# Optimization experiments

Measured on AMD Instinct MI355X. Metric: run time of the kernel, lower is better.

The kernel has to match this reference:

```python
import jax, jax.numpy as jnp
import numpy as np
import math

N_HEADS = 16

def _rope_tables(T, D, dtype):
    # inv_freq over even dims, emb = [freqs, freqs] -> [T, D]
    inv_freq = 1.0 / (10000.0 ** (jnp.arange(0, D, 2, dtype=jnp.float32) / D))
    freqs = jnp.arange(T, dtype=jnp.float32)[:, None] * inv_freq[None, :]  # [T, D/2]
    emb = jnp.concatenate([freqs, freqs], axis=-1)  # [T, D]
    return jnp.cos(emb).astype(dtype), jnp.sin(emb).astype(dtype)

def _rotate_half(x):
    d = x.shape[-1] // 2
    return jnp.concatenate([-x[..., d:], x[..., :d]], axis=-1)

def setup_inputs() -> dict:
    key = jax.random.key(0)
    ks = jax.random.split(key, 5)
    B, T, C = 2, 2048, 1024
    s = 1.0 / math.sqrt(C)
    return {
        "x": jax.random.normal(ks[0], (B, T, C), dtype=jnp.float32),
        "Wq": jax.random.normal(ks[1], (C, C), dtype=jnp.float32) * s,
        "Wk": jax.random.normal(ks[2], (C, C), dtype=jnp.float32) * s,
        "Wv": jax.random.normal(ks[3], (C, C), dtype=jnp.float32) * s,
        "Wo": jax.random.normal(ks[4], (C, C), dtype=jnp.float32) * s,
    }

def reference(x, Wq, Wk, Wv, Wo):
    B, T, C = x.shape
    H = N_HEADS
    D = C // H
    # QKV projections (torch Linear, bias=False: y = x @ W.T), split into heads
    def proj(W):
        return (x @ W.T).reshape(B, T, H, D).transpose(0, 2, 1, 3)  # [B,H,T,D]
    q, k, v = proj(Wq), proj(Wk), proj(Wv)
    # RoPE
    cos, sin = _rope_tables(T, D, x.dtype)  # [T,D] each, broadcast over B,H
    q = q * cos + _rotate_half(q) * sin
    k = k * cos + _rotate_half(k) * sin
    # scaled dot-product attention with causal mask
    scale = 1.0 / math.sqrt(D)
    attn = jnp.einsum('bhtd,bhsd->bhts', q, k) * scale  # [B,H,T,T]
    row = jnp.arange(T)[:, None]
    col = jnp.arange(T)[None, :]
    attn = jnp.where(col > row, -jnp.inf, attn)
    p = jax.nn.softmax(attn, axis=-1)
    out = jnp.einsum('bhts,bhsd->bhtd', p, v)  # [B,H,T,D]
    out = out.transpose(0, 2, 1, 3).reshape(B, T, C)
    return out @ Wo.T
```

## Files before the change

kernel.cpp:

```cpp
#include <hip/hip_runtime.h>
#include <hip/hip_bf16.h>


typedef __hip_bfloat16 bf16;
typedef __attribute__((ext_vector_type(8))) short bf16x8;
typedef __attribute__((ext_vector_type(4))) float f32x4;
typedef __attribute__((ext_vector_type(4))) short short4v;

#define MFMA16(a, b, c) __builtin_amdgcn_mfma_f32_16x16x32_bf16((a), (b), (c), 0, 0, 0)

constexpr int Bn = 2, Hn = 16, Tn = 2048, Dn = 64, Cn = 1024;
constexpr size_t NE = (size_t)Bn * Tn * Cn;
constexpr size_t WE = (size_t)Cn * Cn;
constexpr float QSCALE = 0.125f * 1.44269504088896f;
constexpr int PS = 68;

__device__ inline unsigned short bfbits(float x) {
    bf16 b = __float2bfloat16(x);
    return *(unsigned short*)&b;
}

__device__ inline bf16x8 pack8(f32x4 a, f32x4 b) {
    bf16x8 r;
#pragma unroll
    for (int i = 0; i < 4; ++i) r[i] = (short)bfbits(a[i]);
#pragma unroll
    for (int i = 0; i < 4; ++i) r[4 + i] = (short)bfbits(b[i]);
    return r;
}

__global__ __launch_bounds__(256) void convert_kernel(
    const float* __restrict__ x, const float* __restrict__ wq,
    const float* __restrict__ wk, const float* __restrict__ wv,
    const float* __restrict__ wo, bf16* __restrict__ dst)
{
    int blk = blockIdx.x;
    int lane = threadIdx.x & 63;
    int lx = lane & 15, quad = lane >> 4;
    const float* src;
    size_t doff;
    if (blk < 2048) {
        int frag = blk * 4 + (threadIdx.x >> 6);
        int mt = frag >> 5, kc = frag & 31;
        src = x + (size_t)(mt * 16 + lx) * Cn + kc * 32 + quad * 8;
        doff = (size_t)frag * 512 + lane * 8;
    } else {
        int w = (blk - 2048) >> 9, b = (blk - 2048) & 511;
        const float* s4[4] = {wq, wk, wv, wo};
        int frag = b * 4 + (threadIdx.x >> 6);
        int nb = frag >> 5, kc = frag & 31;
        src = s4[w] + (size_t)(nb * 16 + lx) * Cn + kc * 32 + quad * 8;
        doff = NE + (size_t)w * WE + (size_t)frag * 512 + lane * 8;
    }
    f32x4 a = *(const f32x4*)(src);
    f32x4 b2 = *(const f32x4*)(src + 4);
    *(bf16x8*)(dst + doff) = pack8(a, b2);
}

__global__ __launch_bounds__(256) void gemm_qkv_kernel(
    const bf16* __restrict__ Xf, const bf16* __restrict__ Wbase,
    bf16* __restrict__ Qo, bf16* __restrict__ Ko, bf16* __restrict__ Vo)
{
    const int bm = blockIdx.x, bn = blockIdx.y, wsel = blockIdx.z;
    const bf16* W = Wbase + (size_t)wsel * WE;
    const int tid  = threadIdx.x;
    const int wave = tid >> 6, lane = tid & 63;
    const int lx   = lane & 15, quad = lane >> 4;
    const int wm = wave >> 1, wn = wave & 1;

    const int mt0 = bm * 8 + wm * 4;
    const int nb0 = bn * 8 + wn * 4;
    const bf16* afrag = Xf + (size_t)mt0 * 32 * 512 + (size_t)lane * 8;
    const bf16* wfrag = W + (size_t)nb0 * 32 * 512 + (size_t)lane * 8;

    f32x4 acc[4][4] = {};
    bf16x8 acur[4], bcur[4], anxt[4], bnxt[4];
#pragma unroll
    for (int i = 0; i < 4; ++i) {
        acur[i] = *(const bf16x8*)(afrag + (size_t)i * 32 * 512);
        bcur[i] = *(const bf16x8*)(wfrag + (size_t)i * 32 * 512);
    }
    for (int kc = 0; kc < 32; ++kc) {
        if (kc < 31) {
#pragma unroll
            for (int i = 0; i < 4; ++i) {
                anxt[i] = *(const bf16x8*)(afrag + ((size_t)i * 32 + kc + 1) * 512);
                bnxt[i] = *(const bf16x8*)(wfrag + ((size_t)i * 32 + kc + 1) * 512);
            }
        }
#pragma unroll
        for (int mt = 0; mt < 4; ++mt)
#pragma unroll
            for (int nt = 0; nt < 4; ++nt)
                acc[mt][nt] = MFMA16(acur[mt], bcur[nt], acc[mt][nt]);
#pragma unroll
        for (int i = 0; i < 4; ++i) { acur[i] = anxt[i]; bcur[i] = bnxt[i]; }
    }

    const int h = bn * 2 + wn;
    if (wsel <= 1) {
#pragma unroll
        for (int mt = 0; mt < 4; ++mt)
#pragma unroll
            for (int r = 0; r < 4; ++r) {
                int mg = bm * 128 + wm * 64 + mt * 16 + quad * 4 + r;
                int t  = mg & (Tn - 1);
#pragma unroll
                for (int nt = 0; nt < 2; ++nt) {
                    int d = nt * 16 + lx;
                    float ang = (float)t * __expf(-(float)d * 0.2878231366f);
                    float c, s;
                    __sincosf(ang, &s, &c);
                    float a0 = acc[mt][nt][r], a1 = acc[mt][nt + 2][r];
                    acc[mt][nt][r]     = a0 * c - a1 * s;
                    acc[mt][nt + 2][r] = a1 * c + a0 * s;
                }
            }
    }

#pragma unroll
    for (int mt = 0; mt < 4; ++mt) {
        int mg0 = bm * 128 + wm * 64 + mt * 16 + quad * 4;
        int b = mg0 >> 11, tlo = mg0 & (Tn - 1);
        if (wsel == 0) {
#pragma unroll
            for (int nt = 0; nt < 4; ++nt)
#pragma unroll
                for (int r = 0; r < 4; ++r) {
                    int d = nt * 16 + lx;
                    Qo[((size_t)(b * Hn + h) * Tn + tlo + r) * Dn + d] =
                        __float2bfloat16(acc[mt][nt][r] * QSCALE);
                }
        } else if (wsel == 1) {
            bf16* Kf = Ko + (size_t)(b * Hn + h) * Tn * Dn;
            int c = tlo >> 6, ntk = (tlo >> 4) & 3;
#pragma unroll
            for (int nt = 0; nt < 4; ++nt) {
                size_t base = ((size_t)(c * 4 + ntk) * 2 + (nt >> 1)) * 512
                            + (size_t)((nt & 1) * 2 + (lx >> 3)) * 128
                            + (size_t)(tlo & 15) * 8 + (lx & 7);
#pragma unroll
                for (int r = 0; r < 4; ++r)
                    Kf[base + (size_t)r * 8] = __float2bfloat16(acc[mt][nt][r]);
            }
        } else {
            bf16* Vf = Vo + (size_t)(b * Hn + h) * Tn * Dn;
            int c = tlo >> 6, ksv = (tlo >> 5) & 1;
            int qv = (tlo >> 3) & 3, pos0 = tlo & 7;
#pragma unroll
            for (int nt = 0; nt < 4; ++nt) {
                short4v pk;
#pragma unroll
                for (int r = 0; r < 4; ++r) pk[r] = (short)bfbits(acc[mt][nt][r]);
                *(short4v*)&Vf[((size_t)(c * 8 + nt * 2 + ksv)) * 512
                               + (size_t)qv * 128 + (size_t)lx * 8 + pos0] = pk;
            }
        }
    }
}

__global__ __launch_bounds__(256) void gemm_out_kernel(
    const bf16* __restrict__ Af, const bf16* __restrict__ W, float* __restrict__ Out)
{
    const int bm = blockIdx.x, bn = blockIdx.y;
    const int tid  = threadIdx.x;
    const int wave = tid >> 6, lane = tid & 63;
    const int lx   = lane & 15, quad = lane >> 4;
    const int wm = wave >> 1, wn = wave & 1;

    const int mt0 = bm * 8 + wm * 4;
    const int nb0 = bn * 8 + wn * 4;
    const bf16* afrag = Af + (size_t)mt0 * 32 * 512 + (size_t)lane * 8;
    const bf16* wfrag = W + (size_t)nb0 * 32 * 512 + (size_t)lane * 8;

    f32x4 acc[4][4] = {};
    bf16x8 acur[4], bcur[4], anxt[4], bnxt[4];
#pragma unroll
    for (int i = 0; i < 4; ++i) {
        acur[i] = *(const bf16x8*)(afrag + (size_t)i * 32 * 512);
        bcur[i] = *(const bf16x8*)(wfrag + (size_t)i * 32 * 512);
    }
    for (int kc = 0; kc < 32; ++kc) {
        if (kc < 31) {
#pragma unroll
            for (int i = 0; i < 4; ++i) {
                anxt[i] = *(const bf16x8*)(afrag + ((size_t)i * 32 + kc + 1) * 512);
                bnxt[i] = *(const bf16x8*)(wfrag + ((size_t)i * 32 + kc + 1) * 512);
            }
        }
#pragma unroll
        for (int mt = 0; mt < 4; ++mt)
#pragma unroll
            for (int nt = 0; nt < 4; ++nt)
                acc[mt][nt] = MFMA16(acur[mt], bcur[nt], acc[mt][nt]);
#pragma unroll
        for (int i = 0; i < 4; ++i) { acur[i] = anxt[i]; bcur[i] = bnxt[i]; }
    }
#pragma unroll
    for (int mt = 0; mt < 4; ++mt)
#pragma unroll
        for (int nt = 0; nt < 4; ++nt)
#pragma unroll
            for (int r = 0; r < 4; ++r) {
                int mg = bm * 128 + wm * 64 + mt * 16 + quad * 4 + r;
                int ng = bn * 128 + wn * 64 + nt * 16 + lx;
                Out[(size_t)mg * Cn + ng] = acc[mt][nt][r];
            }
}

__global__ __launch_bounds__(256) void attn_kernel(
    const bf16* __restrict__ Q, const bf16* __restrict__ K,
    const bf16* __restrict__ Vt, bf16* __restrict__ O)
{
    __shared__ unsigned short Pl[4][16 * PS];
    const int f  = blockIdx.x;
    const int bh = (f & 7) * 4 + ((f >> 3) & 3);
    const int qb = 31 - (f >> 5);
    const int tid  = threadIdx.x;
    const int wave = tid >> 6, lane = tid & 63;
    const int lx   = lane & 15, quad = lane >> 4;

    const bf16* Qh = Q  + (size_t)bh * Tn * Dn;
    const bf16* Kh = K  + (size_t)bh * Tn * Dn;
    const bf16* Vh = Vt + (size_t)bh * Tn * Dn;
    unsigned short* pw = &Pl[wave][0];

    const int qrowA = qb * 64 + wave * 16 + lx;
    bf16x8 aq0 = *(const bf16x8*)(Qh + (size_t)qrowA * Dn + quad * 8);
    bf16x8 aq1 = *(const bf16x8*)(Qh + (size_t)qrowA * Dn + 32 + quad * 8);

    bf16x8 ones;
#pragma unroll
    for (int i = 0; i < 8; ++i) ones[i] = (short)0x3F80;

    f32x4 acc_o[4] = {};
    f32x4 acc_l = {};
    const int row_local = wave * 16 + quad * 4;

    auto load8 = [&](bf16x8* d, const bf16* p) {
#pragma unroll
        for (int i = 0; i < 8; ++i) d[i] = *(const bf16x8*)(p + (size_t)i * 512);
    };

    auto step = [&](const bf16x8* k, const bf16* vptr, bool diag) {
        bf16x8 v[8];
#pragma unroll
        for (int i = 0; i < 8; ++i) v[i] = *(const bf16x8*)(vptr + (size_t)i * 512);
        f32x4 accs[4] = {};
#pragma unroll
        for (int nt = 0; nt < 4; ++nt) {
            accs[nt] = MFMA16(aq0, k[nt * 2], accs[nt]);
            accs[nt] = MFMA16(aq1, k[nt * 2 + 1], accs[nt]);
        }
        if (!diag) {
#pragma unroll
            for (int nt = 0; nt < 4; ++nt)
#pragma unroll
                for (int r = 0; r < 4; ++r)
                    pw[(quad * 4 + r) * PS + nt * 16 + lx] = bfbits(exp2f(accs[nt][r]));
        } else {
#pragma unroll
            for (int nt = 0; nt < 4; ++nt) {
                int keyl = nt * 16 + lx;
#pragma unroll
                for (int r = 0; r < 4; ++r) {
                    float p2 = (keyl > row_local + r) ? 0.0f : exp2f(accs[nt][r]);
                    pw[(quad * 4 + r) * PS + nt * 16 + lx] = bfbits(p2);
                }
            }
        }
        asm volatile("s_waitcnt lgkmcnt(0)" ::: "memory");
        bf16x8 ap0 = *(const bf16x8*)&pw[lx * PS + quad * 8];
        bf16x8 ap1 = *(const bf16x8*)&pw[lx * PS + 32 + quad * 8];
        acc_l = MFMA16(ap0, ones, acc_l);
        acc_l = MFMA16(ap1, ones, acc_l);
#pragma unroll
        for (int dt = 0; dt < 4; ++dt) {
            acc_o[dt] = MFMA16(ap0, v[dt * 2], acc_o[dt]);
            acc_o[dt] = MFMA16(ap1, v[dt * 2 + 1], acc_o[dt]);
        }
    };

    const bf16* kp = Kh + lane * 8;
    const bf16* vp = Vh + lane * 8;

    bf16x8 ka[8], kb[8];
    load8(ka, kp);

    int ch = 0;
    while (ch + 1 <= qb) {
        load8(kb, kp + 4096);
        step(ka, vp, false);
        if (ch + 2 <= qb) load8(ka, kp + 8192);
        step(kb, vp + 4096, (ch + 1) == qb);
        kp += 8192; vp += 8192; ch += 2;
    }
    if (ch == qb)
        step(ka, vp, true);

    const int b = bh >> 4, h = bh & 15;
    const int mtile = b * 128 + qb * 4 + wave;
#pragma unroll
    for (int dt = 0; dt < 4; ++dt) {
        int ch2 = h * 64 + dt * 16 + lx;
        size_t base = ((size_t)mtile * 32 + (ch2 >> 5)) * 512
                    + (size_t)(((ch2 >> 3) & 3) * 16) * 8 + (ch2 & 7);
#pragma unroll
        for (int r = 0; r < 4; ++r) {
            float o = acc_o[dt][r] / acc_l[r];
            O[base + (size_t)(quad * 4 + r) * 8] = __float2bfloat16(o);
        }
    }
}

extern "C" void kernel_launch(void* const* d_in, const int* in_sizes, int n_in,
                              void* d_out, int out_size, void* d_ws, size_t ws_size,
                              hipStream_t stream)
{
    const float* x  = (const float*)d_in[0];
    const float* Wq = (const float*)d_in[1];
    const float* Wk = (const float*)d_in[2];
    const float* Wv = (const float*)d_in[3];
    const float* Wo = (const float*)d_in[4];
    float* out = (float*)d_out;

    bf16* ws = (bf16*)d_ws;
    bf16* Xf = ws;
    bf16* Wb = ws + NE;
    bf16* Qb = ws + NE + 4 * WE;
    bf16* Kb = Qb + NE;
    bf16* Vb = Kb + NE;
    bf16* Ab = Xf;

    convert_kernel<<<4096, 256, 0, stream>>>(x, Wq, Wk, Wv, Wo, ws);
    gemm_qkv_kernel<<<dim3(32, 8, 3), 256, 0, stream>>>(Xf, Wb, Qb, Kb, Vb);
    attn_kernel<<<1024, 256, 0, stream>>>(Qb, Kb, Vb, Ab);
    gemm_out_kernel<<<dim3(32, 8), 256, 0, stream>>>(Ab, Wb + 3 * WE, out);
}
```

Baseline: 178.8 us.

## Pair high and low causal query tiles per block to balance work and share K/V

Each attention block now handles two query tiles (p and 31-p) of the same head, so every block does the same amount of causal work and the K/V chunks loaded for the low tile are reused by the high tile. The grid is halved to 512 blocks and launch bounds request 2 blocks per CU. In exchange, the explicit double-buffered K prefetch is removed and per-thread register use rises from the doubled accumulators. Fewer blocks may also reduce latency hiding.

```diff
diff --git a/kernel.cpp b/kernel.cpp
--- a/kernel.cpp
+++ b/kernel.cpp
@@ -208,14 +208,15 @@
             }
 }
 
-__global__ __launch_bounds__(256) void attn_kernel(
+__global__ __launch_bounds__(256, 2) void attn_kernel(
     const bf16* __restrict__ Q, const bf16* __restrict__ K,
     const bf16* __restrict__ Vt, bf16* __restrict__ O)
 {
     __shared__ unsigned short Pl[4][16 * PS];
-    const int f  = blockIdx.x;
-    const int bh = (f & 7) * 4 + ((f >> 3) & 3);
-    const int qb = 31 - (f >> 5);
+    const int g  = blockIdx.x;
+    const int bh = g & 31;
+    const int p  = g >> 5;
+    const int tHi = 31 - p, tLo = p;
     const int tid  = threadIdx.x;
     const int wave = tid >> 6, lane = tid & 63;
     const int lx   = lane & 15, quad = lane >> 4;
@@ -225,33 +226,22 @@
     const bf16* Vh = Vt + (size_t)bh * Tn * Dn;
     unsigned short* pw = &Pl[wave][0];
 
-    const int qrowA = qb * 64 + wave * 16 + lx;
-    bf16x8 aq0 = *(const bf16x8*)(Qh + (size_t)qrowA * Dn + quad * 8);
-    bf16x8 aq1 = *(const bf16x8*)(Qh + (size_t)qrowA * Dn + 32 + quad * 8);
+    const int qrowH = tHi * 64 + wave * 16 + lx;
+    bf16x8 aqH0 = *(const bf16x8*)(Qh + (size_t)qrowH * Dn + quad * 8);
+    bf16x8 aqH1 = *(const bf16x8*)(Qh + (size_t)qrowH * Dn + 32 + quad * 8);
+    const int qrowL = tLo * 64 + wave * 16 + lx;
+    bf16x8 aqL0 = *(const bf16x8*)(Qh + (size_t)qrowL * Dn + quad * 8);
+    bf16x8 aqL1 = *(const bf16x8*)(Qh + (size_t)qrowL * Dn + 32 + quad * 8);
 
     bf16x8 ones;
 #pragma unroll
     for (int i = 0; i < 8; ++i) ones[i] = (short)0x3F80;
 
-    f32x4 acc_o[4] = {};
-    f32x4 acc_l = {};
+    f32x4 acc_oH[4] = {}, acc_oL[4] = {};
+    f32x4 acc_lH = {},    acc_lL = {};
     const int row_local = wave * 16 + quad * 4;
 
-    auto load8 = [&](bf16x8* d, const bf16* p) {
-#pragma unroll
-        for (int i = 0; i < 8; ++i) d[i] = *(const bf16x8*)(p + (size_t)i * 512);
-    };
-
-    auto step = [&](const bf16x8* k, const bf16* vptr, bool diag) {
-        bf16x8 v[8];
-#pragma unroll
-        for (int i = 0; i < 8; ++i) v[i] = *(const bf16x8*)(vptr + (size_t)i * 512);
-        f32x4 accs[4] = {};
-#pragma unroll
-        for (int nt = 0; nt < 4; ++nt) {
-            accs[nt] = MFMA16(aq0, k[nt * 2], accs[nt]);
-            accs[nt] = MFMA16(aq1, k[nt * 2 + 1], accs[nt]);
-        }
+    auto storeP = [&](const f32x4* accs, bool diag) {
         if (!diag) {
 #pragma unroll
             for (int nt = 0; nt < 4; ++nt)
@@ -264,53 +254,82 @@
                 int keyl = nt * 16 + lx;
 #pragma unroll
                 for (int r = 0; r < 4; ++r) {
-                    float p2 = (keyl > row_local + r) ? 0.0f : exp2f(accs[nt][r]);
-                    pw[(quad * 4 + r) * PS + nt * 16 + lx] = bfbits(p2);
+                    float pv = (keyl > row_local + r) ? 0.0f : exp2f(accs[nt][r]);
+                    pw[(quad * 4 + r) * PS + nt * 16 + lx] = bfbits(pv);
                 }
             }
         }
+    };
+
+    for (int c = 0; c <= tHi; ++c) {
+        const bf16* kp = Kh + (size_t)c * 4096 + lane * 8;
+        const bf16* vp = Vh + (size_t)c * 4096 + lane * 8;
+        bf16x8 k[8], v[8];
+#pragma unroll
+        for (int i = 0; i < 8; ++i) {
+            k[i] = *(const bf16x8*)(kp + (size_t)i * 512);
+            v[i] = *(const bf16x8*)(vp + (size_t)i * 512);
+        }
+        const bool lo = (c <= tLo);
+        f32x4 accsH[4] = {};
+#pragma unroll
+        for (int nt = 0; nt < 4; ++nt) {
+            accsH[nt] = MFMA16(aqH0, k[nt * 2], accsH[nt]);
+            accsH[nt] = MFMA16(aqH1, k[nt * 2 + 1], accsH[nt]);
+        }
+        f32x4 accsL[4] = {};
+        if (lo) {
+#pragma unroll
+            for (int nt = 0; nt < 4; ++nt) {
+                accsL[nt] = MFMA16(aqL0, k[nt * 2], accsL[nt]);
+                accsL[nt] = MFMA16(aqL1, k[nt * 2 + 1], accsL[nt]);
+            }
+        }
+        storeP(accsH, c == tHi);
         asm volatile("s_waitcnt lgkmcnt(0)" ::: "memory");
-        bf16x8 ap0 = *(const bf16x8*)&pw[lx * PS + quad * 8];
-        bf16x8 ap1 = *(const bf16x8*)&pw[lx * PS + 32 + quad * 8];
-        acc_l = MFMA16(ap0, ones, acc_l);
-        acc_l = MFMA16(ap1, ones, acc_l);
+        {
+            bf16x8 ap0 = *(const bf16x8*)&pw[lx * PS + quad * 8];
+            bf16x8 ap1 = *(const bf16x8*)&pw[lx * PS + 32 + quad * 8];
+            acc_lH = MFMA16(ap0, ones, acc_lH);
+            acc_lH = MFMA16(ap1, ones, acc_lH);
+#pragma unroll
+            for (int dt = 0; dt < 4; ++dt) {
+                acc_oH[dt] = MFMA16(ap0, v[dt * 2], acc_oH[dt]);
+                acc_oH[dt] = MFMA16(ap1, v[dt * 2 + 1], acc_oH[dt]);
+            }
+        }
+        if (lo) {
+            storeP(accsL, c == tLo);
+            asm volatile("s_waitcnt lgkmcnt(0)" ::: "memory");
+            bf16x8 ap0 = *(const bf16x8*)&pw[lx * PS + quad * 8];
+            bf16x8 ap1 = *(const bf16x8*)&pw[lx * PS + 32 + quad * 8];
+            acc_lL = MFMA16(ap0, ones, acc_lL);
+            acc_lL = MFMA16(ap1, ones, acc_lL);
+#pragma unroll
+            for (int dt = 0; dt < 4; ++dt) {
+                acc_oL[dt] = MFMA16(ap0, v[dt * 2], acc_oL[dt]);
+                acc_oL[dt] = MFMA16(ap1, v[dt * 2 + 1], acc_oL[dt]);
+            }
+        }
+    }
+
+    const int b = bh >> 4, h = bh & 15;
+    auto writeO = [&](int t, const f32x4* acc_o, const f32x4& acc_l) {
+        const int mtile = b * 128 + t * 4 + wave;
 #pragma unroll
         for (int dt = 0; dt < 4; ++dt) {
-            acc_o[dt] = MFMA16(ap0, v[dt * 2], acc_o[dt]);
-            acc_o[dt] = MFMA16(ap1, v[dt * 2 + 1], acc_o[dt]);
+            int ch = h * 64 + dt * 16 + lx;
+            size_t base = ((size_t)mtile * 32 + (ch >> 5)) * 512
+                        + (size_t)(((ch >> 3) & 3) * 16) * 8 + (ch & 7);
+#pragma unroll
+            for (int r = 0; r < 4; ++r) {
+                float o = acc_o[dt][r] / acc_l[r];
+                O[base + (size_t)(quad * 4 + r) * 8] = __float2bfloat16(o);
+            }
         }
     };
-
-    const bf16* kp = Kh + lane * 8;
-    const bf16* vp = Vh + lane * 8;
-
-    bf16x8 ka[8], kb[8];
-    load8(ka, kp);
-
-    int ch = 0;
-    while (ch + 1 <= qb) {
-        load8(kb, kp + 4096);
-        step(ka, vp, false);
-        if (ch + 2 <= qb) load8(ka, kp + 8192);
-        step(kb, vp + 4096, (ch + 1) == qb);
-        kp += 8192; vp += 8192; ch += 2;
-    }
-    if (ch == qb)
-        step(ka, vp, true);
-
-    const int b = bh >> 4, h = bh & 15;
-    const int mtile = b * 128 + qb * 4 + wave;
-#pragma unroll
-    for (int dt = 0; dt < 4; ++dt) {
-        int ch2 = h * 64 + dt * 16 + lx;
-        size_t base = ((size_t)mtile * 32 + (ch2 >> 5)) * 512
-                    + (size_t)(((ch2 >> 3) & 3) * 16) * 8 + (ch2 & 7);
-#pragma unroll
-        for (int r = 0; r < 4; ++r) {
-            float o = acc_o[dt][r] / acc_l[r];
-            O[base + (size_t)(quad * 4 + r) * 8] = __float2bfloat16(o);
-        }
-    }
+    writeO(tHi, acc_oH, acc_lH);
+    writeO(tLo, acc_oL, acc_lL);
 }
 
 extern "C" void kernel_launch(void* const* d_in, const int* in_sizes, int n_in,
@@ -334,6 +353,6 @@
 
     convert_kernel<<<4096, 256, 0, stream>>>(x, Wq, Wk, Wv, Wo, ws);
     gemm_qkv_kernel<<<dim3(32, 8, 3), 256, 0, stream>>>(Xf, Wb, Qb, Kb, Vb);
-    attn_kernel<<<1024, 256, 0, stream>>>(Qb, Kb, Vb, Ab);
+    attn_kernel<<<512, 256, 0, stream>>>(Qb, Kb, Vb, Ab);
     gemm_out_kernel<<<dim3(32, 8), 256, 0, stream>>>(Ab, Wb + 3 * WE, out);
 }
```

After: 178.0 us. About the same (-0.5%).
